# Optimization experiments

Measured on AMD Instinct MI355X. Metric: run time of the kernel, lower is better.

Reference implementation:

```python
import jax, jax.numpy as jnp
import numpy as np

EMBED_DIM = 1024
NUM_HEADS = 16
HEAD_DIM = EMBED_DIM // NUM_HEADS


def setup_inputs() -> dict:
    key = jax.random.key(0)
    k1, k2, k3, k4, k5 = jax.random.split(key, 5)
    B, N, C = 4, 2048, EMBED_DIM
    s = 1.0 / np.sqrt(C)
    return {
        "x": jax.random.normal(k1, (B, N, C), dtype=jnp.float32),
        "w_qkv": jax.random.uniform(k2, (C, 3 * C), dtype=jnp.float32, minval=-s, maxval=s),
        "b_qkv": jax.random.uniform(k3, (3 * C,), dtype=jnp.float32, minval=-s, maxval=s),
        "w_out": jax.random.uniform(k4, (C, C), dtype=jnp.float32, minval=-s, maxval=s),
        "b_out": jax.random.uniform(k5, (C,), dtype=jnp.float32, minval=-s, maxval=s),
    }


def reference(x, w_qkv, b_qkv, w_out, b_out):
    B, N, C = x.shape
    H, D = NUM_HEADS, HEAD_DIM
    qkv = x @ w_qkv + b_qkv                       # [B, N, 3C]
    qkv = qkv.reshape(B, N, 3, H, D)
    q = qkv[:, :, 0].transpose(0, 2, 1, 3)        # [B, H, N, D]
    k = qkv[:, :, 1].transpose(0, 2, 1, 3)
    v = qkv[:, :, 2].transpose(0, 2, 1, 3)
    scale = 1.0 / np.sqrt(D).astype(np.float32)
    attn = jnp.einsum('bhnd,bhmd->bhnm', q, k) * scale  # [B, H, N, N]
    attn = jax.nn.softmax(attn, axis=-1)
    out = jnp.einsum('bhnm,bhmd->bhnd', attn, v)  # [B, H, N, D]
    out = out.transpose(0, 2, 1, 3).reshape(B, N, C)
    return out @ w_out + b_out
```

## Files before the change

kernel.cpp:

```cpp
#include <hip/hip_runtime.h>


typedef unsigned short u16;
typedef unsigned long long u64;
typedef __bf16 bf16x8 __attribute__((ext_vector_type(8)));
typedef float f32x4 __attribute__((ext_vector_type(4)));
typedef unsigned int u32x2 __attribute__((ext_vector_type(2)));

#define MFMA(a, b, c) __builtin_amdgcn_mfma_f32_16x16x32_bf16(a, b, c, 0, 0, 0)

#define QSCALE 0.18033688011112043f

__device__ __forceinline__ u16 f2bf(float f) {
    __bf16 h = (__bf16)f;
    return *(u16*)&h;
}

__device__ __forceinline__ float fexp2(float x) {
#if __has_builtin(__builtin_amdgcn_exp2f)
    return __builtin_amdgcn_exp2f(x);
#else
    return __expf(x * 0.6931471805599453f);
#endif
}

__device__ __forceinline__ void gld16(const void* g, void* l) {
    __builtin_amdgcn_global_load_lds(
        (const __attribute__((address_space(1))) void*)g,
        (__attribute__((address_space(3))) void*)l, 16, 0, 0);
}

__global__ __launch_bounds__(256) void cvt_f32_bf16(
    const float* __restrict__ src, u16* __restrict__ dst, long n)
{
    long i = ((long)blockIdx.x * 256 + threadIdx.x) * 8;
    if (i >= n) return;
    float4 a = *(const float4*)&src[i];
    float4 b = *(const float4*)&src[i + 4];
    union { u16 u[8]; uint4 v; } tmp;
    tmp.u[0] = f2bf(a.x); tmp.u[1] = f2bf(a.y);
    tmp.u[2] = f2bf(a.z); tmp.u[3] = f2bf(a.w);
    tmp.u[4] = f2bf(b.x); tmp.u[5] = f2bf(b.y);
    tmp.u[6] = f2bf(b.z); tmp.u[7] = f2bf(b.w);
    *(uint4*)&dst[i] = tmp.v;
}

__global__ __launch_bounds__(256) void transpose_f2b(
    const float* __restrict__ src, u16* __restrict__ dst, int R, int C)
{
    __shared__ alignas(16) u16 tile[64 * 80];
    const int r0 = blockIdx.y * 64, c0 = blockIdx.x * 64;
    const int t = threadIdx.x;
#pragma unroll
    for (int c = 0; c < 4; c++) {
        int idx = t + c * 256;
        int r = idx >> 4, seg = idx & 15;
        float4 f = *(const float4*)&src[(long)(r0 + r) * C + c0 + seg * 4];
        u16* p = &tile[r * 80 + seg * 4];
        p[0] = f2bf(f.x); p[1] = f2bf(f.y); p[2] = f2bf(f.z); p[3] = f2bf(f.w);
    }
    __syncthreads();
#pragma unroll
    for (int c = 0; c < 2; c++) {
        int idx = t + c * 256;
        int rr = idx >> 3, seg = idx & 7;
        union { u16 u[8]; uint4 v; } tmp;
#pragma unroll
        for (int j = 0; j < 8; j++) tmp.u[j] = tile[(seg * 8 + j) * 80 + rr];
        *(uint4*)&dst[(long)(c0 + rr) * R + r0 + seg * 8] = tmp.v;
    }
}

template <int EPI>
__global__ __launch_bounds__(256) void gemm_bf16(
    const u16* __restrict__ A, const u16* __restrict__ Bt,
    const float* __restrict__ bias,
    u16* __restrict__ out0, u16* __restrict__ out1, u16* __restrict__ out2,
    float* __restrict__ outf,
    int M, int N, int K)
{
    const int m0 = blockIdx.x * 128, n0 = blockIdx.y * 128;
    const int t = threadIdx.x;
    const int wave = t >> 6, lane = t & 63, quad = lane >> 4, l15 = lane & 15;
    const int wm = wave >> 1, wn = wave & 1;

    __shared__ alignas(16) u16 As[128 * 64];
    __shared__ alignas(16) u16 Bs[128 * 64];

    const int srow = wave * 32 + (lane >> 3);
    const int scol = (((lane & 7) ^ (lane >> 3)) & 7) * 8;

    f32x4 acc[4][4] = {};

    for (int k0 = 0; k0 < K; k0 += 64) {
        __syncthreads();
#pragma unroll
        for (int c = 0; c < 4; c++) {
            gld16(&A[(long)(m0 + srow + c * 8) * K + k0 + scol],
                  &As[(wave * 32 + c * 8) * 64]);
            gld16(&Bt[(long)(n0 + srow + c * 8) * K + k0 + scol],
                  &Bs[(wave * 32 + c * 8) * 64]);
        }
        __syncthreads();

#pragma unroll
        for (int ks = 0; ks < 2; ks++) {
            bf16x8 af[4], bf[4];
#pragma unroll
            for (int mt = 0; mt < 4; mt++) {
                int row = wm * 64 + mt * 16 + l15;
                af[mt] = *(bf16x8*)&As[row * 64 + (((ks * 4 + quad) ^ (row & 7)) * 8)];
            }
#pragma unroll
            for (int nt = 0; nt < 4; nt++) {
                int row = wn * 64 + nt * 16 + l15;
                bf[nt] = *(bf16x8*)&Bs[row * 64 + (((ks * 4 + quad) ^ (row & 7)) * 8)];
            }
#pragma unroll
            for (int mt = 0; mt < 4; mt++)
#pragma unroll
                for (int nt = 0; nt < 4; nt++)
                    acc[mt][nt] = MFMA(bf[nt], af[mt], acc[mt][nt]);
        }
    }

#pragma unroll
    for (int mt = 0; mt < 4; mt++) {
        int token = m0 + wm * 64 + mt * 16 + l15;
        int bb = token >> 11, nn = token & 2047;
#pragma unroll
        for (int nt = 0; nt < 4; nt++) {
            int cgb = n0 + wn * 64 + nt * 16 + quad * 4;
            float4 bv = *(const float4*)&bias[cgb];
            float v0 = acc[mt][nt][0] + bv.x;
            float v1 = acc[mt][nt][1] + bv.y;
            float v2 = acc[mt][nt][2] + bv.z;
            float v3 = acc[mt][nt][3] + bv.w;
            if (EPI == 0) {
                int t3 = cgb >> 10;
                int hh = (cgb >> 6) & 15, dd = cgb & 63;
                int bh = (bb << 4) + hh;
                if (t3 == 0) {
                    union { u16 u[4]; u64 v; } pk;
                    pk.u[0] = f2bf(v0 * QSCALE); pk.u[1] = f2bf(v1 * QSCALE);
                    pk.u[2] = f2bf(v2 * QSCALE); pk.u[3] = f2bf(v3 * QSCALE);
                    *(u64*)&out0[((long)bh * 2048 + nn) * 64 + dd] = pk.v;
                } else if (t3 == 1) {
                    union { u16 u[4]; u64 v; } pk;
                    pk.u[0] = f2bf(v0); pk.u[1] = f2bf(v1);
                    pk.u[2] = f2bf(v2); pk.u[3] = f2bf(v3);
                    *(u64*)&out1[((long)bh * 2048 + nn) * 64 + dd] = pk.v;
                } else {
                    long vbo = ((long)bh * 64 + dd) * 2048 + nn;
                    out2[vbo]            = f2bf(v0);
                    out2[vbo + 2048]     = f2bf(v1);
                    out2[vbo + 2 * 2048] = f2bf(v2);
                    out2[vbo + 3 * 2048] = f2bf(v3);
                }
            } else {
                float4 o4 = { v0, v1, v2, v3 };
                *(float4*)&outf[(long)token * N + cgb] = o4;
            }
        }
    }
}

__global__ __launch_bounds__(256, 2) void flash_attn(
    const u16* __restrict__ q, const u16* __restrict__ k,
    const u16* __restrict__ vt, u16* __restrict__ attn)
{
    const int bh = blockIdx.x;
    const int b = bh >> 4, h = bh & 15;
    const int q0 = blockIdx.y * 256;
    const int t = threadIdx.x;
    const int wave = t >> 6, lane = t & 63, quad = lane >> 4, l15 = lane & 15;

    __shared__ alignas(16) u16 Ks[2][4096];
    __shared__ alignas(16) u16 Vs[2][4096];

    const u16* kb = k + (long)bh * 2048 * 64;
    const u16* vb = vt + (long)bh * 64 * 2048;

    bf16x8 qf[4][2];
#pragma unroll
    for (int mt = 0; mt < 4; mt++) {
        long row = (long)bh * 2048 + q0 + wave * 64 + mt * 16 + l15;
        qf[mt][0] = *(const bf16x8*)&q[row * 64 + quad * 8];
        qf[mt][1] = *(const bf16x8*)&q[row * 64 + 32 + quad * 8];
    }

    bf16x8 ones;
#pragma unroll
    for (int j = 0; j < 8; j++) ones[j] = (__bf16)1.0f;

    const int ri = lane >> 3;
    const int ci = (lane & 7) ^ ri;
    const int sg = wave * 2;

    const int lperm = (l15 & 3) | ((l15 & 4) << 1) | ((l15 & 8) >> 1);
    const int swk = (quad ^ (lperm & 7)) * 8;
    const int swv = (quad ^ (l15 & 7)) * 8;

    const int koff0 = lperm * 64 + swk;
    const int koff1 = lperm * 64 + (swk ^ 32);
    const int voff[2] = { l15 * 64 + swv, l15 * 64 + (swv ^ 32) };

    f32x4 o[4][4] = {};
    f32x4 ls[4] = {};

    const u16* kp0 = kb + (long)((sg + 0) * 8 + ri) * 64 + ci * 8;
    const u16* kp1 = kb + (long)((sg + 1) * 8 + ri) * 64 + ci * 8;
    const u16* vp0 = vb + (long)((sg + 0) * 8 + ri) * 2048 + ci * 8;
    const u16* vp1 = vb + (long)((sg + 1) * 8 + ri) * 2048 + ci * 8;

    gld16(kp0, &Ks[0][(sg + 0) * 512]);
    gld16(kp1, &Ks[0][(sg + 1) * 512]);
    gld16(vp0, &Vs[0][(sg + 0) * 512]);
    gld16(vp1, &Vs[0][(sg + 1) * 512]);
    kp0 += 4096; kp1 += 4096; vp0 += 64; vp1 += 64;

    for (int kt2 = 0; kt2 < 16; kt2++) {
#pragma unroll
        for (int half = 0; half < 2; half++) {
            const int cur = half;
            const bool stage_next = (half == 0) | (kt2 < 15);

            __syncthreads();

            if (stage_next) {
                gld16(kp0, &Ks[cur ^ 1][(sg + 0) * 512]);
                gld16(kp1, &Ks[cur ^ 1][(sg + 1) * 512]);
                gld16(vp0, &Vs[cur ^ 1][(sg + 0) * 512]);
                gld16(vp1, &Vs[cur ^ 1][(sg + 1) * 512]);
                kp0 += 4096; kp1 += 4096; vp0 += 64; vp1 += 64;
            }

            f32x4 st[4][4];
            __builtin_amdgcn_s_setprio(1);
#pragma unroll
            for (int ct = 0; ct < 4; ct++) {
                bf16x8 kf0 = *(const bf16x8*)&Ks[cur][ct * 1024 + koff0];
                bf16x8 kf1 = *(const bf16x8*)&Ks[cur][ct * 1024 + koff1];
#pragma unroll
                for (int mt = 0; mt < 4; mt++) {
                    f32x4 z = {};
                    z = MFMA(kf0, qf[mt][0], z);
                    st[mt][ct] = MFMA(kf1, qf[mt][1], z);
                }
            }
            __builtin_amdgcn_s_setprio(0);

#pragma unroll
            for (int hp = 0; hp < 2; hp++) {
                bf16x8 va[4];
#pragma unroll
                for (int dt = 0; dt < 4; dt++)
                    va[dt] = *(const bf16x8*)&Vs[cur][dt * 1024 + voff[hp]];

                bf16x8 pb[4];
#pragma unroll
                for (int mt = 0; mt < 4; mt++) {
                    unsigned w[2][2];
#pragma unroll
                    for (int c = 0; c < 2; c++)
#pragma unroll
                        for (int p = 0; p < 2; p++) {
                            u16 lo = f2bf(fexp2(st[mt][2 * hp + c][2 * p]));
                            u16 hi = f2bf(fexp2(st[mt][2 * hp + c][2 * p + 1]));
                            w[c][p] = (unsigned)lo | ((unsigned)hi << 16);
                        }
                    u32x2 pa0 = __builtin_amdgcn_permlane32_swap(
                        w[0][0], w[1][0], false, false);
                    u32x2 pa1 = __builtin_amdgcn_permlane32_swap(
                        w[0][1], w[1][1], false, false);
                    union { unsigned d[4]; bf16x8 v; } uu;
                    uu.d[0] = pa0[0];
                    uu.d[1] = pa1[0];
                    uu.d[2] = pa0[1];
                    uu.d[3] = pa1[1];
                    pb[mt] = uu.v;
                }

                __builtin_amdgcn_s_setprio(1);
#pragma unroll
                for (int mt = 0; mt < 4; mt++)
                    ls[mt] = MFMA(ones, pb[mt], ls[mt]);
#pragma unroll
                for (int dt = 0; dt < 4; dt++)
#pragma unroll
                    for (int mt = 0; mt < 4; mt++)
                        o[mt][dt] = MFMA(va[dt], pb[mt], o[mt][dt]);
                __builtin_amdgcn_s_setprio(0);
            }
        }
    }

#pragma unroll
    for (int mt = 0; mt < 4; mt++) {
        float inv = 1.f / ls[mt][0];
        int n = q0 + wave * 64 + mt * 16 + l15;
#pragma unroll
        for (int dt = 0; dt < 4; dt++) {
            union { u16 u[4]; u64 v; } pk;
#pragma unroll
            for (int r = 0; r < 4; r++) pk.u[r] = f2bf(o[mt][dt][r] * inv);
            *(u64*)&attn[((long)b * 2048 + n) * 1024 + h * 64 + dt * 16 + quad * 4] =
                pk.v;
        }
    }
}

extern "C" void kernel_launch(void* const* d_in, const int* in_sizes, int n_in,
                              void* d_out, int out_size, void* d_ws, size_t ws_size,
                              hipStream_t stream) {
    const float* x     = (const float*)d_in[0];
    const float* w_qkv = (const float*)d_in[1];
    const float* b_qkv = (const float*)d_in[2];
    const float* w_out = (const float*)d_in[3];
    const float* b_out = (const float*)d_in[4];
    float* out = (float*)d_out;

    u16* ws    = (u16*)d_ws;
    u16* q     = ws;
    u16* kk    = q + 8388608;
    u16* vt    = kk + 8388608;
    u16* attn  = vt + 8388608;
    u16* x_bf  = attn + 8388608;
    u16* wqkvT = x_bf + 8388608;
    u16* woutT = wqkvT + 3145728;

    cvt_f32_bf16<<<4096, 256, 0, stream>>>(x, x_bf, 8388608L);
    transpose_f2b<<<dim3(48, 16), 256, 0, stream>>>(w_qkv, wqkvT, 1024, 3072);
    transpose_f2b<<<dim3(16, 16), 256, 0, stream>>>(w_out, woutT, 1024, 1024);
    gemm_bf16<0><<<dim3(64, 24), 256, 0, stream>>>(x_bf, wqkvT, b_qkv, q, kk, vt,
                                                   nullptr, 8192, 3072, 1024);
    flash_attn<<<dim3(64, 8), 256, 0, stream>>>(q, kk, vt, attn);
    gemm_bf16<1><<<dim3(64, 8), 256, 0, stream>>>(attn, woutT, b_out, nullptr,
                                                  nullptr, nullptr, out,
                                                  8192, 1024, 1024);
}
```

Before: 258.7 us.

## Triple-buffer GEMM LDS loads and enlarge tiles to 256x128 with 512 threads

Rewrites the bf16 GEMM main loop as a three-stage LDS pipeline. Global-to-LDS loads for tile k+2 are issued while tile k is being computed, with explicit vmcnt waits and raw s_barrier instead of two __syncthreads per tile. The block grows to 512 threads covering a 256x128 tile, and MFMA sections run at raised wave priority. The aim is to hide global load latency and cut barrier stalls, at the cost of much more LDS (about 144KB), one block per CU, and halved grid sizes.

```diff
diff --git a/kernel.cpp b/kernel.cpp
--- a/kernel.cpp
+++ b/kernel.cpp
@@ -29,6 +29,10 @@
         (const __attribute__((address_space(1))) void*)g,
         (__attribute__((address_space(3))) void*)l, 16, 0, 0);
 }
+
+__device__ __forceinline__ void bar()      { __asm__ volatile("s_barrier" ::: "memory"); }
+__device__ __forceinline__ void wait_vm6() { __asm__ volatile("s_waitcnt vmcnt(6)" ::: "memory"); }
+__device__ __forceinline__ void wait_vm0() { __asm__ volatile("s_waitcnt vmcnt(0)" ::: "memory"); }
 
 __global__ __launch_bounds__(256) void cvt_f32_bf16(
     const float* __restrict__ src, u16* __restrict__ dst, long n)
@@ -72,57 +76,91 @@
 }
 
 template <int EPI>
-__global__ __launch_bounds__(256) void gemm_bf16(
+__global__ __launch_bounds__(512, 1) void gemm_bf16(
     const u16* __restrict__ A, const u16* __restrict__ Bt,
     const float* __restrict__ bias,
     u16* __restrict__ out0, u16* __restrict__ out1, u16* __restrict__ out2,
     float* __restrict__ outf,
     int M, int N, int K)
 {
-    const int m0 = blockIdx.x * 128, n0 = blockIdx.y * 128;
+    const int m0 = blockIdx.x * 256, n0 = blockIdx.y * 128;
     const int t = threadIdx.x;
     const int wave = t >> 6, lane = t & 63, quad = lane >> 4, l15 = lane & 15;
     const int wm = wave >> 1, wn = wave & 1;
 
-    __shared__ alignas(16) u16 As[128 * 64];
-    __shared__ alignas(16) u16 Bs[128 * 64];
-
-    const int srow = wave * 32 + (lane >> 3);
-    const int scol = (((lane & 7) ^ (lane >> 3)) & 7) * 8;
+    __shared__ alignas(16) u16 As[3][16384];
+    __shared__ alignas(16) u16 Bs[3][8192];
+
+    const int sr = lane >> 3;
+    const int sc8 = ((lane & 7) ^ sr) * 8;
+
+    const int rx = l15 & 7;
+    int arow[4], brow[4];
+#pragma unroll
+    for (int ft = 0; ft < 4; ft++) {
+        arow[ft] = (wm * 64 + ft * 16 + l15) * 64;
+        brow[ft] = (wn * 64 + ft * 16 + l15) * 64;
+    }
+    const int xoff[2] = { ((0 * 4 + quad) ^ rx) * 8, ((1 * 4 + quad) ^ rx) * 8 };
+
+    const int NT = K >> 6;
+
+#define STAGE_A(kt_, slot_, o_)                                               \
+    gld16(&A[(long)(m0 + (o_) * 64 + wave * 8 + sr) * K + ((kt_) << 6) + sc8],\
+          &As[slot_][(o_) * 4096 + wave * 512])
+#define STAGE_B(kt_, slot_, o_)                                               \
+    gld16(&Bt[(long)(n0 + (o_) * 64 + wave * 8 + sr) * K + ((kt_) << 6) + sc8],\
+          &Bs[slot_][(o_) * 4096 + wave * 512])
+
+#pragma unroll
+    for (int s = 0; s < 2; s++) {
+        STAGE_A(s, s, 0); STAGE_A(s, s, 1); STAGE_A(s, s, 2); STAGE_A(s, s, 3);
+        STAGE_B(s, s, 0); STAGE_B(s, s, 1);
+    }
+    wait_vm6();
+    bar();
 
     f32x4 acc[4][4] = {};
-
-    for (int k0 = 0; k0 < K; k0 += 64) {
-        __syncthreads();
-#pragma unroll
-        for (int c = 0; c < 4; c++) {
-            gld16(&A[(long)(m0 + srow + c * 8) * K + k0 + scol],
-                  &As[(wave * 32 + c * 8) * 64]);
-            gld16(&Bt[(long)(n0 + srow + c * 8) * K + k0 + scol],
-                  &Bs[(wave * 32 + c * 8) * 64]);
-        }
-        __syncthreads();
+    int cur = 0, c2 = 2;
+
+    for (int kt = 0; kt < NT; kt++) {
+        const u16* Ac = As[cur];
+        const u16* Bc = Bs[cur];
+        const bool st = (kt + 2 < NT);
 
 #pragma unroll
         for (int ks = 0; ks < 2; ks++) {
             bf16x8 af[4], bf[4];
 #pragma unroll
-            for (int mt = 0; mt < 4; mt++) {
-                int row = wm * 64 + mt * 16 + l15;
-                af[mt] = *(bf16x8*)&As[row * 64 + (((ks * 4 + quad) ^ (row & 7)) * 8)];
-            }
-#pragma unroll
-            for (int nt = 0; nt < 4; nt++) {
-                int row = wn * 64 + nt * 16 + l15;
-                bf[nt] = *(bf16x8*)&Bs[row * 64 + (((ks * 4 + quad) ^ (row & 7)) * 8)];
-            }
+            for (int ft = 0; ft < 4; ft++) {
+                af[ft] = *(const bf16x8*)&Ac[arow[ft] + xoff[ks]];
+                bf[ft] = *(const bf16x8*)&Bc[brow[ft] + xoff[ks]];
+            }
+            if (st) {
+                if (ks == 0) { STAGE_A(kt + 2, c2, 0); STAGE_A(kt + 2, c2, 1);
+                               STAGE_A(kt + 2, c2, 2); }
+                else         { STAGE_A(kt + 2, c2, 3);
+                               STAGE_B(kt + 2, c2, 0); STAGE_B(kt + 2, c2, 1); }
+            }
+            bar();
+            __builtin_amdgcn_s_setprio(1);
 #pragma unroll
             for (int mt = 0; mt < 4; mt++)
 #pragma unroll
                 for (int nt = 0; nt < 4; nt++)
                     acc[mt][nt] = MFMA(bf[nt], af[mt], acc[mt][nt]);
+            __builtin_amdgcn_s_setprio(0);
+            if (ks == 1) {
+                if (st)               wait_vm6();
+                else if (kt + 1 < NT) wait_vm0();
+            }
+            bar();
         }
-    }
+        cur = (cur == 2) ? 0 : cur + 1;
+        c2  = (c2 == 2) ? 0 : c2 + 1;
+    }
+#undef STAGE_A
+#undef STAGE_B
 
 #pragma unroll
     for (int mt = 0; mt < 4; mt++) {
@@ -332,10 +370,10 @@
     cvt_f32_bf16<<<4096, 256, 0, stream>>>(x, x_bf, 8388608L);
     transpose_f2b<<<dim3(48, 16), 256, 0, stream>>>(w_qkv, wqkvT, 1024, 3072);
     transpose_f2b<<<dim3(16, 16), 256, 0, stream>>>(w_out, woutT, 1024, 1024);
-    gemm_bf16<0><<<dim3(64, 24), 256, 0, stream>>>(x_bf, wqkvT, b_qkv, q, kk, vt,
+    gemm_bf16<0><<<dim3(32, 24), 512, 0, stream>>>(x_bf, wqkvT, b_qkv, q, kk, vt,
                                                    nullptr, 8192, 3072, 1024);
     flash_attn<<<dim3(64, 8), 256, 0, stream>>>(q, kk, vt, attn);
-    gemm_bf16<1><<<dim3(64, 8), 256, 0, stream>>>(attn, woutT, b_out, nullptr,
+    gemm_bf16<1><<<dim3(32, 8), 512, 0, stream>>>(attn, woutT, b_out, nullptr,
                                                   nullptr, nullptr, out,
                                                   8192, 1024, 1024);
 }
```

Result: slower. 269.1 us (+4.0%).
